# Performance work log

Measured on AMD Instinct MI355X. Metric: run time of the kernel, lower is better.

The kernel has to match this reference:

```python
import jax, jax.numpy as jnp
import numpy as np

B, S, D, M = 8, 4096, 1024, 32
W_SCALE = 0.03  # keep gate pre-activations in a sane range


def setup_inputs() -> dict:
    key = jax.random.key(0)
    ks = jax.random.split(key, 7)
    return {
        "x": jax.random.normal(ks[0], (B, S, D), dtype=jnp.float32),
        "Wr": jax.random.normal(ks[1], (D, M), dtype=jnp.float32) * W_SCALE,
        "br": jnp.zeros((M,), dtype=jnp.float32),
        "Ww": jax.random.normal(ks[2], (D, M), dtype=jnp.float32) * W_SCALE,
        "bw": jnp.zeros((M,), dtype=jnp.float32),
        "Wm": jax.random.normal(ks[3], (D, M), dtype=jnp.float32) * W_SCALE,
        "bm": jnp.zeros((M,), dtype=jnp.float32),
        "Wp": jax.random.normal(ks[4], (M, D), dtype=jnp.float32) * W_SCALE,
        "bp": jnp.zeros((D,), dtype=jnp.float32),
        "Wo": jax.random.normal(ks[5], (2 * D, D), dtype=jnp.float32) * W_SCALE,
        "bo": jnp.zeros((D,), dtype=jnp.float32),
    }


def _forward(x, Wr, br, Ww, bw, Wm, bm, Wp, bp, Wo, bo):
    Bd, Sd, Dd = x.shape
    Md = Wr.shape[1]
    # All input-only linears are state-independent: batch them as big GEMMs.
    read_w = jax.nn.sigmoid(jnp.einsum("bsd,dm->bsm", x, Wr) + br)   # [B,S,M]
    write_w = jax.nn.sigmoid(jnp.einsum("bsd,dm->bsm", x, Ww) + bw)  # [B,S,M]
    new_mem = jnp.einsum("bsd,dm->bsm", x, Wm) + bm                  # [B,S,M]
    # Split output_gate weight: cat([x_t, mv]) @ Wo == x_t @ Wo_x + mv @ Wo_m
    Wo_x, Wo_m = Wo[:Dd], Wo[Dd:]
    pre_x = jnp.einsum("bsd,de->bse", x, Wo_x) + bo                  # [B,S,D]

    def step(mem, inp):
        r, w, nm, px = inp  # [B,M],[B,M],[B,M],[B,D]
        mv = (r * mem) @ Wp + bp                 # memory_proj(read * state)
        fused = jnp.tanh(px + mv @ Wo_m)         # output_gate(cat([x_t, mv]))
        mem_new = jax.lax.stop_gradient((1.0 - w) * mem + w * nm)  # .detach()
        return mem_new, fused

    mem0 = jnp.zeros((Bd, Md), dtype=x.dtype)
    xs = (
        jnp.swapaxes(read_w, 0, 1),
        jnp.swapaxes(write_w, 0, 1),
        jnp.swapaxes(new_mem, 0, 1),
        jnp.swapaxes(pre_x, 0, 1),
    )
    _, outs = jax.lax.scan(step, mem0, xs)  # outs: [S,B,D]
    return jnp.swapaxes(outs, 0, 1)         # [B,S,D]


def reference(x, Wr, br, Ww, bw, Wm, bm, Wp, bp, Wo, bo):
    return _forward(x, Wr, br, Ww, bw, Wm, bm, Wp, bp, Wo, bo)
```

## Files before the change

kernel.cpp:

```cpp
#include <hip/hip_runtime.h>

typedef unsigned short u16;
typedef __bf16 bf16x8 __attribute__((ext_vector_type(8)));
typedef float f32x4 __attribute__((ext_vector_type(4)));

#define BS_TOT 32768
#define SS 4096
#define DD 1024
#define MM 32

__device__ __forceinline__ float bf2f(u16 u) {
    union { float f; unsigned int i; } c; c.i = ((unsigned int)u) << 16; return c.f;
}
__device__ __forceinline__ u16 f2bf(float f) {
    union { float f; unsigned int i; } c; c.f = f;
    unsigned int r = c.i + 0x7FFFu + ((c.i >> 16) & 1u);
    return (u16)(r >> 16);
}
__device__ __forceinline__ f32x4 mfma16(bf16x8 a, bf16x8 b, f32x4 c) {
    return __builtin_amdgcn_mfma_f32_16x16x32_bf16(a, b, c, 0, 0, 0);
}
__device__ __forceinline__ u16 cvt_in(const void* p, size_t i, int f32m) {
    return f32m ? f2bf(((const float*)p)[i]) : ((const u16*)p)[i];
}
__device__ __forceinline__ uint4 pack8(float4 a, float4 b) {
    uint4 v;
    v.x = (unsigned)f2bf(a.x) | ((unsigned)f2bf(a.y) << 16);
    v.y = (unsigned)f2bf(a.z) | ((unsigned)f2bf(a.w) << 16);
    v.z = (unsigned)f2bf(b.x) | ((unsigned)f2bf(b.y) << 16);
    v.w = (unsigned)f2bf(b.z) | ((unsigned)f2bf(b.w) << 16);
    return v;
}
__device__ __forceinline__ void gload16(u16* l, const u16* g) {
    __builtin_amdgcn_global_load_lds(
        (const __attribute__((address_space(1))) unsigned int*)(g),
        (__attribute__((address_space(3))) unsigned int*)(l),
        16, 0, 0);
}

__global__ __launch_bounds__(64) void zej_detect(const unsigned int* __restrict__ xw,
                                                 int* __restrict__ flag)
{
    int lane = threadIdx.x;
    int cnt = 0;
#pragma unroll
    for (int i = 0; i < 16; i++) {
        unsigned int w = xw[lane * 16 + i];
        unsigned int e = (w >> 7) & 0xFFu;
        cnt += (e >= 110u && e <= 135u) ? 1 : 0;
    }
#pragma unroll
    for (int off = 32; off > 0; off >>= 1) cnt += __shfl_down(cnt, off);
    if (lane == 0) *flag = (cnt < 512) ? 1 : 0;
}

__global__ __launch_bounds__(256) void zej_pack(
    const void* __restrict__ Wr, const void* __restrict__ Ww, const void* __restrict__ Wm,
    const void* __restrict__ Wo,
    const void* __restrict__ br, const void* __restrict__ bw, const void* __restrict__ bm,
    u16* __restrict__ W3T, u16* __restrict__ WoxT, u16* __restrict__ biasp,
    const int* __restrict__ flag)
{
    const int f32m = *flag;
    int i = blockIdx.x * 256 + threadIdx.x;
    if (i < 98304) {
        int j = i >> 10, k = i & 1023;
        W3T[i] = (j < 32) ? cvt_in(Wr, (size_t)k * 32 + j, f32m)
               : (j < 64) ? cvt_in(Ww, (size_t)k * 32 + (j - 32), f32m)
                          : cvt_in(Wm, (size_t)k * 32 + (j - 64), f32m);
        return;
    }
    i -= 98304;
    if (i < 1048576) {
        int n = i >> 10, k = i & 1023;
        WoxT[i] = cvt_in(Wo, (size_t)k * 1024 + n, f32m);
        return;
    }
    i -= 1048576;
    if (i < 96) {
        biasp[i] = (i < 32) ? cvt_in(br, i, f32m)
                 : (i < 64) ? cvt_in(bw, i - 32, f32m)
                            : cvt_in(bm, i - 64, f32m);
    }
}

__global__ __launch_bounds__(256) void zej_wpm_a(
    const void* __restrict__ Wp, const void* __restrict__ Wo,
    const void* __restrict__ bp,
    float* __restrict__ part, const int* __restrict__ flag)
{
    __shared__ float wpc[64 * 33];
    __shared__ float bpc[64];
    const int f32m = *flag;
    const int t = threadIdx.x;
    const int nb = blockIdx.x & 15;
    const int kb = blockIdx.x >> 4;
    const int d0 = kb * 64;

    for (int i = t; i < 2048; i += 256) {
        int m = i >> 6, dd = i & 63;
        float v = f32m ? ((const float*)Wp)[m * 1024 + d0 + dd]
                       : bf2f(((const u16*)Wp)[m * 1024 + d0 + dd]);
        wpc[dd * 33 + m] = v;
    }
    if (t < 64)
        bpc[t] = f32m ? ((const float*)bp)[d0 + t] : bf2f(((const u16*)bp)[d0 + t]);
    __syncthreads();

    const int n = nb * 64 + (t & 63);
    const int g = t >> 6;
    float acc[8];
#pragma unroll
    for (int j = 0; j < 8; j++) acc[j] = 0.f;
    float bacc = 0.f;

    for (int dd = 0; dd < 64; dd++) {
        float w = f32m ? ((const float*)Wo)[(size_t)(1024 + d0 + dd) * 1024 + n]
                       : bf2f(((const u16*)Wo)[(size_t)(1024 + d0 + dd) * 1024 + n]);
        const float* wp8 = &wpc[dd * 33 + g * 8];
#pragma unroll
        for (int j = 0; j < 8; j++) acc[j] += wp8[j] * w;
        if (g == 0) bacc += bpc[dd] * w;
    }
    float* pk = part + (size_t)kb * 33792;
#pragma unroll
    for (int j = 0; j < 8; j++) pk[(g * 8 + j) * 1024 + n] = acc[j];
    if (g == 0) pk[32 * 1024 + n] = bacc;
}

__global__ __launch_bounds__(256) void zej_wpm_b(
    const float* __restrict__ part, const void* __restrict__ bo,
    u16* __restrict__ WpmT, float* __restrict__ bpm, const int* __restrict__ flag)
{
    const int f32m = *flag;
    const int t = threadIdx.x;
    const int bid = blockIdx.x;
    if (bid < 128) {
        int m = bid >> 2;
        int n = (bid & 3) * 256 + t;
        float acc = 0.f;
#pragma unroll
        for (int kb = 0; kb < 16; kb++) acc += part[(size_t)kb * 33792 + m * 1024 + n];
        WpmT[(size_t)n * 32 + m] = f2bf(acc);
    } else {
        int n = (bid - 128) * 256 + t;
        float acc = 0.f;
#pragma unroll
        for (int kb = 0; kb < 16; kb++) acc += part[(size_t)kb * 33792 + 32 * 1024 + n];
        float b = f32m ? ((const float*)bo)[n] : bf2f(((const u16*)bo)[n]);
        bpm[n] = acc + b;
    }
}

__global__ __launch_bounds__(256) void zej_gates(
    const void* __restrict__ x, const u16* __restrict__ W3T,
    const u16* __restrict__ biasp, u16* __restrict__ gates,
    u16* __restrict__ xb, const int* __restrict__ flag)
{
    __shared__ __align__(16) u16 As[128][88];
    __shared__ __align__(16) u16 Bs[96][88];
    const int f32m = *flag;
    const int t = threadIdx.x;
    const int lane = t & 63;
    const int wv = t >> 6;
    const int row0 = blockIdx.x * 128;
    const int lm = lane & 15, lq = lane >> 4;

    f32x4 acc[2][6];
    f32x4 z = {0.f, 0.f, 0.f, 0.f};
#pragma unroll
    for (int i = 0; i < 2; i++)
#pragma unroll
        for (int j = 0; j < 6; j++) acc[i][j] = z;

    for (int k0 = 0; k0 < 1024; k0 += 64) {
#pragma unroll
        for (int c = 0; c < 4; c++) {
            int chunk = t + c * 256;
            int r = chunk >> 3, kc = (chunk & 7) * 8;
            size_t gi = (size_t)(row0 + r) * 1024 + k0 + kc;
            uint4 v;
            if (f32m) {
                const float* xf = (const float*)x;
                float4 f0 = *(const float4*)(xf + gi);
                float4 f1 = *(const float4*)(xf + gi + 4);
                v = pack8(f0, f1);
            } else {
                v = *(const uint4*)((const u16*)x + gi);
            }
            *(uint4*)&As[r][kc] = v;
            *(uint4*)(xb + gi) = v;
        }
#pragma unroll
        for (int c = 0; c < 3; c++) {
            int chunk = t + c * 256;
            int j = chunk >> 3, kc = (chunk & 7) * 8;
            *(uint4*)&Bs[j][kc] = *(const uint4*)&W3T[j * 1024 + k0 + kc];
        }
        __syncthreads();
#pragma unroll
        for (int ks = 0; ks < 2; ks++) {
            int kk = ks * 32 + lq * 8;
            bf16x8 a[2], b[6];
#pragma unroll
            for (int rt = 0; rt < 2; rt++) a[rt] = *(const bf16x8*)&As[wv * 32 + rt * 16 + lm][kk];
#pragma unroll
            for (int ct = 0; ct < 6; ct++) b[ct] = *(const bf16x8*)&Bs[ct * 16 + lm][kk];
#pragma unroll
            for (int rt = 0; rt < 2; rt++)
#pragma unroll
                for (int ct = 0; ct < 6; ct++)
                    acc[rt][ct] = mfma16(a[rt], b[ct], acc[rt][ct]);
        }
        __syncthreads();
    }
#pragma unroll
    for (int rt = 0; rt < 2; rt++) {
#pragma unroll
        for (int ct = 0; ct < 6; ct++) {
            int col = ct * 16 + lm;
            float bias = bf2f(biasp[col]);
            bool sig = (col < 64);
#pragma unroll
            for (int p = 0; p < 4; p++) {
                int R = row0 + wv * 32 + rt * 16 + lq * 4 + p;
                float v = acc[rt][ct][p] + bias;
                if (sig) v = 1.f / (1.f + __expf(-v));
                gates[R * 96 + col] = f2bf(v);
            }
        }
    }
}

__global__ __launch_bounds__(64) void zej_scan(
    const u16* __restrict__ gates, u16* __restrict__ rm)
{
    const int c = blockIdx.x;
    const int b = c >> 5;
    const int m = c & 31;
    const int lane = threadIdx.x;
    const u16* gb = gates + (size_t)b * SS * 96;
    const int tbase = lane * 64;

    float A = 1.f, Bc = 0.f;
    for (int i = 0; i < 64; i++) {
        int idx = (tbase + i) * 96;
        float w = bf2f(gb[idx + 32 + m]);
        float nm = bf2f(gb[idx + 64 + m]);
        float a = 1.f - w;
        Bc = a * Bc + w * nm;
        A *= a;
    }
    for (int off = 1; off < 64; off <<= 1) {
        float Ap = __shfl_up(A, off);
        float Bp = __shfl_up(Bc, off);
        if (lane >= off) { Bc = A * Bp + Bc; A = A * Ap; }
    }
    float Bprev = __shfl_up(Bc, 1);
    float mem = (lane == 0) ? 0.f : Bprev;

    for (int i = 0; i < 64; i++) {
        int idx = (tbase + i) * 96;
        float r = bf2f(gb[idx + m]);
        float w = bf2f(gb[idx + 32 + m]);
        float nm = bf2f(gb[idx + 64 + m]);
        rm[((size_t)b * SS + tbase + i) * 32 + m] = f2bf(r * mem);
        mem = (1.f - w) * mem + w * nm;
    }
}

__global__ __launch_bounds__(256) void zej_out(
    const u16* __restrict__ xb, const u16* __restrict__ rm,
    const u16* __restrict__ WoxT, const u16* __restrict__ WpmT,
    const float* __restrict__ bpm, float* __restrict__ out)
{
    __shared__ __align__(16) u16 As[128 * 64];
    __shared__ __align__(16) u16 Bs[128 * 64];
    const int t = threadIdx.x;
    const int lane = t & 63;
    const int wv = t >> 6;
    const int wr = (wv >> 1) * 64;
    const int wc = (wv & 1) * 64;
    const int row0 = blockIdx.x * 128;
    const int n0 = blockIdx.y * 128;
    const int lm = lane & 15, lq = lane >> 4;

    f32x4 acc[4][4];
    f32x4 z = {0.f, 0.f, 0.f, 0.f};
#pragma unroll
    for (int i = 0; i < 4; i++)
#pragma unroll
        for (int j = 0; j < 4; j++) acc[i][j] = z;

    const int sr = lane >> 3;
    const int slot = lane & 7;
    const int kcs = 8 * (slot ^ sr);

    for (int k0 = 0; k0 < 1024; k0 += 64) {
#pragma unroll
        for (int i = 0; i < 4; i++) {
            int ra = (wv * 4 + i) * 8 + sr;
            gload16(&As[(wv * 4 + i) * 512], xb   + (size_t)(row0 + ra) * 1024 + k0 + kcs);
            gload16(&Bs[(wv * 4 + i) * 512], WoxT + (size_t)(n0  + ra) * 1024 + k0 + kcs);
        }
        __syncthreads();
#pragma unroll
        for (int ks = 0; ks < 2; ks++) {
            bf16x8 a[4], b[4];
#pragma unroll
            for (int rt = 0; rt < 4; rt++) {
                int R = wr + rt * 16 + lm;
                int cb = (ks * 64 + lq * 16) ^ ((R & 7) << 4);
                a[rt] = *(const bf16x8*)((const char*)As + R * 128 + cb);
            }
#pragma unroll
            for (int ct = 0; ct < 4; ct++) {
                int R = wc + ct * 16 + lm;
                int cb = (ks * 64 + lq * 16) ^ ((R & 7) << 4);
                b[ct] = *(const bf16x8*)((const char*)Bs + R * 128 + cb);
            }
#pragma unroll
            for (int rt = 0; rt < 4; rt++)
#pragma unroll
                for (int ct = 0; ct < 4; ct++)
                    acc[rt][ct] = mfma16(a[rt], b[ct], acc[rt][ct]);
        }
        __syncthreads();
    }

    {
        const int sr2 = lane >> 2;
        const int slot2 = lane & 3;
        const int kcs2 = 8 * (slot2 ^ (sr2 & 3));
#pragma unroll
        for (int i = 0; i < 2; i++) {
            int ra = (wv * 2 + i) * 16 + sr2;
            gload16(&As[(wv * 2 + i) * 512], rm   + (size_t)(row0 + ra) * 32 + kcs2);
            gload16(&Bs[(wv * 2 + i) * 512], WpmT + (size_t)(n0  + ra) * 32 + kcs2);
        }
        __syncthreads();
        bf16x8 a[4], b[4];
#pragma unroll
        for (int rt = 0; rt < 4; rt++) {
            int R = wr + rt * 16 + lm;
            a[rt] = *(const bf16x8*)((const char*)As + R * 64 + ((lq * 16) ^ ((R & 3) << 4)));
        }
#pragma unroll
        for (int ct = 0; ct < 4; ct++) {
            int R = wc + ct * 16 + lm;
            b[ct] = *(const bf16x8*)((const char*)Bs + R * 64 + ((lq * 16) ^ ((R & 3) << 4)));
        }
#pragma unroll
        for (int rt = 0; rt < 4; rt++)
#pragma unroll
            for (int ct = 0; ct < 4; ct++)
                acc[rt][ct] = mfma16(a[rt], b[ct], acc[rt][ct]);
    }

#pragma unroll
    for (int rt = 0; rt < 4; rt++) {
#pragma unroll
        for (int ct = 0; ct < 4; ct++) {
            int n = n0 + wc + ct * 16 + lm;
            float bias = bpm[n];
#pragma unroll
            for (int p = 0; p < 4; p++) {
                int R = row0 + wr + rt * 16 + lq * 4 + p;
                float v = acc[rt][ct][p] + bias;
                float e = __expf(2.f * v);
                out[(size_t)R * 1024 + n] = 1.f - 2.f / (e + 1.f);
            }
        }
    }
}

extern "C" void kernel_launch(void* const* d_in, const int* in_sizes, int n_in,
                              void* d_out, int out_size, void* d_ws, size_t ws_size,
                              hipStream_t stream)
{
    const void* x  = d_in[0];
    const void* Wr = d_in[1];
    const void* br = d_in[2];
    const void* Ww = d_in[3];
    const void* bw = d_in[4];
    const void* Wm = d_in[5];
    const void* bm = d_in[6];
    const void* Wp = d_in[7];
    const void* bp = d_in[8];
    const void* Wo = d_in[9];
    const void* bo = d_in[10];
    float* out = (float*)d_out;

    char* ws = (char*)d_ws;
    int* flag   = (int*)ws;
    u16* W3T    = (u16*)(ws + 1024);
    u16* WoxT   = (u16*)(ws + 197632);
    u16* WpmT   = (u16*)(ws + 2294784);
    u16* biasp  = (u16*)(ws + 2360320);
    float* bpm  = (float*)(ws + 2361344);
    u16* gates  = (u16*)(ws + 2365440);
    u16* rm     = (u16*)(ws + 8656896);
    u16* xb     = (u16*)(ws + 10754048);
    float* Wpm_part = (float*)(ws + 2365440);

    zej_detect<<<1, 64, 0, stream>>>((const unsigned int*)x, flag);
    zej_pack<<<4481, 256, 0, stream>>>(Wr, Ww, Wm, Wo, br, bw, bm,
                                       W3T, WoxT, biasp, flag);
    zej_wpm_a<<<256, 256, 0, stream>>>(Wp, Wo, bp, Wpm_part, flag);
    zej_wpm_b<<<132, 256, 0, stream>>>(Wpm_part, bo, WpmT, bpm, flag);
    zej_gates<<<BS_TOT / 128, 256, 0, stream>>>(x, W3T, biasp, gates, xb, flag);
    zej_scan<<<256, 64, 0, stream>>>(gates, rm);
    zej_out<<<dim3(BS_TOT / 128, 8), 256, 0, stream>>>(xb, rm, WoxT, WpmT, bpm, out);
}
```

Baseline: 450.2 us.

## Transpose gate layout, widen scan to 256 threads, tile Wo transpose, remap out grid

Several changes land together. The gates buffer becomes column-major so the scan can load contiguous 16-element vectors per thread, and the scan now runs 256 threads per channel with a two-level wave/block prefix combine instead of 64 lanes doing strided scalar loads. A new kernel transposes the scan output back to row-major for the output GEMM. The Wo transpose moves into an LDS-tiled kernel so reads and writes coalesce, f32-to-bf16 packing uses hardware conversion, and the output GEMM grid is linearised with a swizzled block order for better L2 reuse. The cost is an extra launch and an extra pass over the scan output.

```diff
diff --git a/kernel.cpp b/kernel.cpp
--- a/kernel.cpp
+++ b/kernel.cpp
@@ -2,6 +2,7 @@
 
 typedef unsigned short u16;
 typedef __bf16 bf16x8 __attribute__((ext_vector_type(8)));
+typedef __bf16 bf16x2 __attribute__((ext_vector_type(2)));
 typedef float f32x4 __attribute__((ext_vector_type(4)));
 
 #define BS_TOT 32768
@@ -23,12 +24,14 @@
 __device__ __forceinline__ u16 cvt_in(const void* p, size_t i, int f32m) {
     return f32m ? f2bf(((const float*)p)[i]) : ((const u16*)p)[i];
 }
-__device__ __forceinline__ uint4 pack8(float4 a, float4 b) {
+__device__ __forceinline__ unsigned cvt2(float x, float y) {
+    bf16x2 p; p[0] = (__bf16)x; p[1] = (__bf16)y;
+    union { bf16x2 v; unsigned u; } c; c.v = p; return c.u;
+}
+__device__ __forceinline__ uint4 pack8c(float4 a, float4 b) {
     uint4 v;
-    v.x = (unsigned)f2bf(a.x) | ((unsigned)f2bf(a.y) << 16);
-    v.y = (unsigned)f2bf(a.z) | ((unsigned)f2bf(a.w) << 16);
-    v.z = (unsigned)f2bf(b.x) | ((unsigned)f2bf(b.y) << 16);
-    v.w = (unsigned)f2bf(b.z) | ((unsigned)f2bf(b.w) << 16);
+    v.x = cvt2(a.x, a.y); v.y = cvt2(a.z, a.w);
+    v.z = cvt2(b.x, b.y); v.w = cvt2(b.z, b.w);
     return v;
 }
 __device__ __forceinline__ void gload16(u16* l, const u16* g) {
@@ -37,6 +40,13 @@
         (__attribute__((address_space(3))) unsigned int*)(l),
         16, 0, 0);
 }
+__device__ __forceinline__ unsigned u4get(const uint4& v, int idx) {
+    return idx == 0 ? v.x : idx == 1 ? v.y : idx == 2 ? v.z : v.w;
+}
+__device__ __forceinline__ u16 elem16(const uint4& a, const uint4& b, int j) {
+    unsigned w = (j < 8) ? u4get(a, j >> 1) : u4get(b, (j - 8) >> 1);
+    return (u16)((j & 1) ? (w >> 16) : (w & 0xFFFFu));
+}
 
 __global__ __launch_bounds__(64) void zej_detect(const unsigned int* __restrict__ xw,
                                                  int* __restrict__ flag)
@@ -56,10 +66,8 @@
 
 __global__ __launch_bounds__(256) void zej_pack(
     const void* __restrict__ Wr, const void* __restrict__ Ww, const void* __restrict__ Wm,
-    const void* __restrict__ Wo,
     const void* __restrict__ br, const void* __restrict__ bw, const void* __restrict__ bm,
-    u16* __restrict__ W3T, u16* __restrict__ WoxT, u16* __restrict__ biasp,
-    const int* __restrict__ flag)
+    u16* __restrict__ W3T, u16* __restrict__ biasp, const int* __restrict__ flag)
 {
     const int f32m = *flag;
     int i = blockIdx.x * 256 + threadIdx.x;
@@ -71,16 +79,34 @@
         return;
     }
     i -= 98304;
-    if (i < 1048576) {
-        int n = i >> 10, k = i & 1023;
-        WoxT[i] = cvt_in(Wo, (size_t)k * 1024 + n, f32m);
-        return;
-    }
-    i -= 1048576;
     if (i < 96) {
         biasp[i] = (i < 32) ? cvt_in(br, i, f32m)
                  : (i < 64) ? cvt_in(bw, i - 32, f32m)
                             : cvt_in(bm, i - 64, f32m);
+    }
+}
+
+__global__ __launch_bounds__(256) void zej_packT(
+    const void* __restrict__ Wo, u16* __restrict__ WoxT, const int* __restrict__ flag)
+{
+    __shared__ float tile[64][65];
+    const int f32m = *flag;
+    const int t = threadIdx.x;
+    const int kb = blockIdx.x & 15, nb = blockIdx.x >> 4;
+    const int k0 = kb * 64, n0 = nb * 64;
+#pragma unroll
+    for (int i = 0; i < 16; i++) {
+        int idx = i * 256 + t;
+        int r = idx >> 6, c = idx & 63;
+        size_t gi = (size_t)(k0 + r) * 1024 + n0 + c;
+        tile[r][c] = f32m ? ((const float*)Wo)[gi] : bf2f(((const u16*)Wo)[gi]);
+    }
+    __syncthreads();
+#pragma unroll
+    for (int i = 0; i < 16; i++) {
+        int idx = i * 256 + t;
+        int nn = idx >> 6, kk = idx & 63;
+        WoxT[(size_t)(n0 + nn) * 1024 + k0 + kk] = f2bf(tile[kk][nn]);
     }
 }
 
@@ -154,7 +180,7 @@
 
 __global__ __launch_bounds__(256) void zej_gates(
     const void* __restrict__ x, const u16* __restrict__ W3T,
-    const u16* __restrict__ biasp, u16* __restrict__ gates,
+    const u16* __restrict__ biasp, u16* __restrict__ gtc,
     u16* __restrict__ xb, const int* __restrict__ flag)
 {
     __shared__ __align__(16) u16 As[128][88];
@@ -184,7 +210,7 @@
                 const float* xf = (const float*)x;
                 float4 f0 = *(const float4*)(xf + gi);
                 float4 f1 = *(const float4*)(xf + gi + 4);
-                v = pack8(f0, f1);
+                v = pack8c(f0, f1);
             } else {
                 v = *(const uint4*)((const u16*)x + gi);
             }
@@ -226,46 +252,98 @@
                 int R = row0 + wv * 32 + rt * 16 + lq * 4 + p;
                 float v = acc[rt][ct][p] + bias;
                 if (sig) v = 1.f / (1.f + __expf(-v));
-                gates[R * 96 + col] = f2bf(v);
+                gtc[(size_t)col * BS_TOT + R] = f2bf(v);
             }
         }
     }
 }
 
-__global__ __launch_bounds__(64) void zej_scan(
-    const u16* __restrict__ gates, u16* __restrict__ rm)
-{
+__global__ __launch_bounds__(256) void zej_scan(
+    const u16* __restrict__ gtc, u16* __restrict__ rmc)
+{
+    __shared__ float sA[4], sB[4];
     const int c = blockIdx.x;
     const int b = c >> 5;
     const int m = c & 31;
-    const int lane = threadIdx.x;
-    const u16* gb = gates + (size_t)b * SS * 96;
-    const int tbase = lane * 64;
+    const int t = threadIdx.x;
+    const int lane = t & 63;
+    const int wv = t >> 6;
+    const size_t base = (size_t)b * SS;
+    const u16* gr  = gtc + (size_t)( 0 + m) * BS_TOT + base;
+    const u16* gw  = gtc + (size_t)(32 + m) * BS_TOT + base;
+    const u16* gnm = gtc + (size_t)(64 + m) * BS_TOT + base;
+    const int i0 = t * 16;
+
+    uint4 w0 = *(const uint4*)(gw + i0);
+    uint4 w1 = *(const uint4*)(gw + i0 + 8);
+    uint4 n0 = *(const uint4*)(gnm + i0);
+    uint4 n1 = *(const uint4*)(gnm + i0 + 8);
 
     float A = 1.f, Bc = 0.f;
-    for (int i = 0; i < 64; i++) {
-        int idx = (tbase + i) * 96;
-        float w = bf2f(gb[idx + 32 + m]);
-        float nm = bf2f(gb[idx + 64 + m]);
+#pragma unroll
+    for (int j = 0; j < 16; j++) {
+        float w  = bf2f(elem16(w0, w1, j));
+        float nm = bf2f(elem16(n0, n1, j));
         float a = 1.f - w;
         Bc = a * Bc + w * nm;
         A *= a;
     }
+    float Ai = A, Bi = Bc;
     for (int off = 1; off < 64; off <<= 1) {
-        float Ap = __shfl_up(A, off);
-        float Bp = __shfl_up(Bc, off);
-        if (lane >= off) { Bc = A * Bp + Bc; A = A * Ap; }
-    }
-    float Bprev = __shfl_up(Bc, 1);
-    float mem = (lane == 0) ? 0.f : Bprev;
-
-    for (int i = 0; i < 64; i++) {
-        int idx = (tbase + i) * 96;
-        float r = bf2f(gb[idx + m]);
-        float w = bf2f(gb[idx + 32 + m]);
-        float nm = bf2f(gb[idx + 64 + m]);
-        rm[((size_t)b * SS + tbase + i) * 32 + m] = f2bf(r * mem);
+        float Ap = __shfl_up(Ai, off);
+        float Bp = __shfl_up(Bi, off);
+        if (lane >= off) { Bi = Ai * Bp + Bi; Ai = Ai * Ap; }
+    }
+    if (lane == 63) { sA[wv] = Ai; sB[wv] = Bi; }
+    __syncthreads();
+    float Aw = 1.f, Bw = 0.f;
+    for (int k = 0; k < wv; k++) {
+        float a2 = sA[k];
+        Bw = a2 * Bw + sB[k];
+        Aw = Aw * a2;
+    }
+    float Ae = __shfl_up(Ai, 1);
+    float Be = __shfl_up(Bi, 1);
+    if (lane == 0) { Ae = 1.f; Be = 0.f; }
+    float mem = Ae * Bw + Be;
+
+    uint4 r0 = *(const uint4*)(gr + i0);
+    uint4 r1 = *(const uint4*)(gr + i0 + 8);
+    u16 o[16];
+#pragma unroll
+    for (int j = 0; j < 16; j++) {
+        float r  = bf2f(elem16(r0, r1, j));
+        float w  = bf2f(elem16(w0, w1, j));
+        float nm = bf2f(elem16(n0, n1, j));
+        o[j] = f2bf(r * mem);
         mem = (1.f - w) * mem + w * nm;
+    }
+    u16* dst = rmc + (size_t)m * BS_TOT + base + i0;
+    *(uint4*)dst       = *(uint4*)&o[0];
+    *(uint4*)(dst + 8) = *(uint4*)&o[8];
+}
+
+__global__ __launch_bounds__(256) void zej_rmt(
+    const u16* __restrict__ rmc, u16* __restrict__ rm)
+{
+    __shared__ __align__(16) u16 tile[32][136];
+    const int t = threadIdx.x;
+    const int R0 = blockIdx.x * 128;
+#pragma unroll
+    for (int c = 0; c < 2; c++) {
+        int idx = t + c * 256;
+        int m = idx >> 4, kq = (idx & 15) * 8;
+        *(uint4*)&tile[m][kq] = *(const uint4*)&rmc[(size_t)m * BS_TOT + R0 + kq];
+    }
+    __syncthreads();
+#pragma unroll
+    for (int c = 0; c < 2; c++) {
+        int idx = t + c * 256;
+        int r = idx & 127, mq = (idx >> 7) * 8;
+        u16 tmp[8];
+#pragma unroll
+        for (int j = 0; j < 8; j++) tmp[j] = tile[mq + j][r];
+        *(uint4*)&rm[(size_t)(R0 + r) * 32 + mq] = *(uint4*)tmp;
     }
 }
 
@@ -281,8 +359,10 @@
     const int wv = t >> 6;
     const int wr = (wv >> 1) * 64;
     const int wc = (wv & 1) * 64;
-    const int row0 = blockIdx.x * 128;
-    const int n0 = blockIdx.y * 128;
+    const int bid = blockIdx.x;
+    const int lin = (bid & 7) * 256 + (bid >> 3);
+    const int row0 = (lin >> 3) * 128;
+    const int n0 = (lin & 7) * 128;
     const int lm = lane & 15, lq = lane >> 4;
 
     f32x4 acc[4][4];
@@ -398,17 +478,19 @@
     u16* WpmT   = (u16*)(ws + 2294784);
     u16* biasp  = (u16*)(ws + 2360320);
     float* bpm  = (float*)(ws + 2361344);
-    u16* gates  = (u16*)(ws + 2365440);
-    u16* rm     = (u16*)(ws + 8656896);
-    u16* xb     = (u16*)(ws + 10754048);
+    u16* gtc    = (u16*)(ws + 2365440);
+    u16* rmc    = (u16*)(ws + 8656896);
+    u16* rm     = (u16*)(ws + 10754048);
+    u16* xb     = (u16*)(ws + 12851200);
     float* Wpm_part = (float*)(ws + 2365440);
 
     zej_detect<<<1, 64, 0, stream>>>((const unsigned int*)x, flag);
-    zej_pack<<<4481, 256, 0, stream>>>(Wr, Ww, Wm, Wo, br, bw, bm,
-                                       W3T, WoxT, biasp, flag);
+    zej_pack<<<385, 256, 0, stream>>>(Wr, Ww, Wm, br, bw, bm, W3T, biasp, flag);
+    zej_packT<<<256, 256, 0, stream>>>(Wo, WoxT, flag);
     zej_wpm_a<<<256, 256, 0, stream>>>(Wp, Wo, bp, Wpm_part, flag);
     zej_wpm_b<<<132, 256, 0, stream>>>(Wpm_part, bo, WpmT, bpm, flag);
-    zej_gates<<<BS_TOT / 128, 256, 0, stream>>>(x, W3T, biasp, gates, xb, flag);
-    zej_scan<<<256, 64, 0, stream>>>(gates, rm);
-    zej_out<<<dim3(BS_TOT / 128, 8), 256, 0, stream>>>(xb, rm, WoxT, WpmT, bpm, out);
-}
+    zej_gates<<<BS_TOT / 128, 256, 0, stream>>>(x, W3T, biasp, gtc, xb, flag);
+    zej_scan<<<256, 256, 0, stream>>>(gtc, rmc);
+    zej_rmt<<<256, 256, 0, stream>>>(rmc, rm);
+    zej_out<<<2048, 256, 0, stream>>>(xb, rm, WoxT, WpmT, bpm, out);
+}
```

New measurement: 409.2 us. 9.1% less time.
